# Kernel optimization log

Hardware: AMD Instinct MI355X
Metric: run time of the kernel (lower is better)

Reference implementation:

```python
import jax, jax.numpy as jnp
import numpy as np


def _safe_norm(x, eps=1e-8):
    return jnp.sqrt(jnp.clip(jnp.sum(x * x, axis=-1, keepdims=True), eps))


def _normalize(x, eps=1e-8):
    return x / _safe_norm(x, eps)


def _safe_direction(primary, fallback, eps=1e-6):
    bad = _safe_norm(primary, eps) < eps  # [N,1] bool
    out = jnp.where(bad, fallback, primary)
    return _normalize(out, eps)


def _build_frames(x):
    # x: [N,3] (N >= 2). Returns per-node rotation frames [N,3,3] (columns = axes).
    d = x[1:] - x[:-1]
    prev = jnp.concatenate([d[:1], d], axis=0)
    nxt = jnp.concatenate([d, d[-1:]], axis=0)
    tangent = _safe_direction(prev + nxt, nxt)
    curvature = _safe_direction(nxt - prev, prev)
    ay_raw = curvature - tangent * jnp.sum(curvature * tangent, axis=-1, keepdims=True)
    ay = _safe_direction(ay_raw, jnp.cross(tangent, prev))
    az = _safe_direction(jnp.cross(tangent, ay), jnp.cross(tangent, curvature))
    ay = _safe_direction(jnp.cross(az, tangent), ay)
    return jnp.stack([tangent, ay, az], axis=-1)


def setup_inputs() -> dict:
    key = jax.random.key(0)
    N, H, EH = 1024, 256, 128  # EH = max(16, H//2)
    ks = jax.random.split(key, 16)

    def lin(k, fi, fo):
        k1, k2 = jax.random.split(k)
        lim = 1.0 / np.sqrt(fi)
        W = jax.random.uniform(k1, (fi, fo), minval=-lim, maxval=lim, dtype=jnp.float32)
        b = jax.random.uniform(k2, (fo,), minval=-lim, maxval=lim, dtype=jnp.float32)
        return W, b

    h = jax.random.normal(ks[0], (N, H), dtype=jnp.float32)
    x_cond = jnp.cumsum(jax.random.normal(ks[1], (N, 3), dtype=jnp.float32) * 1.5, axis=0)
    x_t = x_cond + 0.05 * jax.random.normal(ks[2], (N, 3), dtype=jnp.float32)
    tau = jax.random.uniform(ks[3], (1,), dtype=jnp.float32)
    W_np1, b_np1 = lin(ks[4], H + 6, H)
    W_np2, b_np2 = lin(ks[5], H, H)
    w_src, b_src = lin(ks[6], H, 1)
    w_dst, b_dst = lin(ks[7], H, 1)
    w_ns, b_ns = lin(ks[8], H, 1)
    W_eg1, b_eg1 = lin(ks[9], 4, EH)
    w_eg2, b_eg2 = lin(ks[10], EH, 1)
    W_out1, b_out1 = lin(ks[11], H + 6, H)
    W_out2, b_out2 = lin(ks[12], H, 3)
    return dict(h=h, x_t=x_t, x_cond=x_cond, tau=tau,
                W_np1=W_np1, b_np1=b_np1, W_np2=W_np2, b_np2=b_np2,
                w_src=w_src, b_src=b_src, w_dst=w_dst, b_dst=b_dst,
                w_ns=w_ns, b_ns=b_ns, W_eg1=W_eg1, b_eg1=b_eg1,
                w_eg2=w_eg2, b_eg2=b_eg2, W_out1=W_out1, b_out1=b_out1,
                W_out2=W_out2, b_out2=b_out2)


def reference(h, x_t, x_cond, tau,
              W_np1, b_np1, W_np2, b_np2,
              w_src, b_src, w_dst, b_dst,
              w_ns, b_ns, W_eg1, b_eg1, w_eg2, b_eg2,
              W_out1, b_out1, W_out2, b_out2):
    silu = jax.nn.silu
    n = x_t.shape[0]
    frames = _build_frames(x_cond)                       # [N,3,3]
    delta = x_t - x_cond
    delta_local = jnp.einsum('nji,nj->ni', frames, delta)  # frames^T @ delta
    t = tau.reshape(())
    t_emb = jnp.broadcast_to(jnp.stack([t, jnp.sin(t), jnp.cos(t)]), (n, 3))
    node_feat = jnp.concatenate([h, delta_local, t_emb], axis=-1)
    nh = silu(node_feat @ W_np1 + b_np1)
    nh = silu(nh @ W_np2 + b_np2)                        # [N,H]
    # pairwise local geometry: rel[n,m] = x[m] - x[n], rotated into node n's frame
    rel = x_t[None, :, :] - x_t[:, None, :]              # [N,N,3]
    rel_local = jnp.einsum('nji,nmj->nmi', frames, rel)  # [N,N,3]
    dist = jnp.linalg.norm(rel_local, axis=-1, keepdims=True)
    edge_feat = jnp.concatenate([rel_local, dist], axis=-1)  # [N,N,4]
    eh = silu(edge_feat @ W_eg1 + b_eg1)                 # [N,N,EH]
    edge_logit = (eh @ w_eg2 + b_eg2)[..., 0]            # [N,N]
    src = nh @ w_src + b_src                             # [N,1] -> broadcast over m
    dst = (nh @ w_dst + b_dst)[:, 0]                     # [N]
    logits = src + dst[None, :] + edge_logit             # [N,N]
    diag = jnp.eye(n, dtype=bool)
    logits = jnp.where(diag, -10000.0, logits)
    attn = jax.nn.softmax(logits, axis=1)
    attn = jnp.where(diag, 0.0, attn)
    attn = attn / jnp.clip(jnp.sum(attn, axis=1, keepdims=True), 1e-6)
    ns = jax.nn.sigmoid(nh @ w_ns + b_ns)[:, 0]          # [N]
    msgs = jnp.einsum('nm,m,nmi->ni', attn, ns, rel_local)  # [N,3]
    uf = jnp.concatenate([nh, delta_local, msgs], axis=-1)
    local_update = silu(uf @ W_out1 + b_out1) @ W_out2 + b_out2
    vel_local = local_update + 0.25 * msgs
    return jnp.einsum('nij,nj->ni', frames, vel_local)
```

## Files before the change

kernel.cpp:

```cpp
#include <hip/hip_runtime.h>
#include <math.h>

#define DEV __device__ __forceinline__

typedef float v2f __attribute__((ext_vector_type(2)));
DEV v2f splat2(float s){ return (v2f){s, s}; }
DEV v2f pkfma(v2f a, v2f b, v2f c){ return __builtin_elementwise_fma(a, b, c); }

struct F3 { float x, y, z; };

DEV F3 mkf3(float x, float y, float z){ F3 r; r.x=x; r.y=y; r.z=z; return r; }
DEV F3 f3add(F3 a, F3 b){ return mkf3(a.x+b.x, a.y+b.y, a.z+b.z); }
DEV F3 f3sub(F3 a, F3 b){ return mkf3(a.x-b.x, a.y-b.y, a.z-b.z); }
DEV F3 f3scale(F3 a, float s){ return mkf3(a.x*s, a.y*s, a.z*s); }
DEV float f3dot(F3 a, F3 b){ return a.x*b.x + a.y*b.y + a.z*b.z; }
DEV F3 f3cross(F3 a, F3 b){
  return mkf3(a.y*b.z - a.z*b.y, a.z*b.x - a.x*b.z, a.x*b.y - a.y*b.x);
}
DEV F3 f3dir(F3 v){
  float ss = f3dot(v, v);
  float inv = 1.0f / sqrtf(fmaxf(ss, 1e-6f));
  return f3scale(v, inv);
}
DEV float fast_silu(float x){
  return x * __builtin_amdgcn_rcpf(1.0f + __expf(-x));
}
DEV float fast_sigmoid(float x){
  return __builtin_amdgcn_rcpf(1.0f + __expf(-x));
}

__global__ __launch_bounds__(256) void node_mlp(
    const float* __restrict__ h, const float* __restrict__ xc,
    const float* __restrict__ xt, const float* __restrict__ tau,
    const float* __restrict__ W1, const float* __restrict__ b1,
    const float* __restrict__ W2, const float* __restrict__ b2,
    const float* __restrict__ w_src, const float* __restrict__ b_src,
    const float* __restrict__ w_dst, const float* __restrict__ b_dst,
    const float* __restrict__ w_ns, const float* __restrict__ b_ns,
    const float* __restrict__ W_eg1, const float* __restrict__ b_eg1,
    const float* __restrict__ w_eg2,
    float* __restrict__ frames, float* __restrict__ dl,
    float* __restrict__ wpk,
    float* __restrict__ nh, float* __restrict__ srcv,
    float* __restrict__ dstv, float* __restrict__ nsv, int N)
{
  const int n0 = blockIdx.x * 4, tid = threadIdx.x;
  __shared__ float4 fA[262];
  __shared__ float4 fB[256];
  __shared__ float red[4][4][3];
  __shared__ float sdl[4][3];

  if (blockIdx.x == 0 && tid >= 128) {
    int j = tid - 128;
    const float nl2e = -1.44269504088896340736f;
    const float nln2 = -0.69314718055994530942f;
    wpk[j*8+0] = nl2e * W_eg1[j];
    wpk[j*8+1] = nl2e * W_eg1[128 + j];
    wpk[j*8+2] = nl2e * W_eg1[256 + j];
    wpk[j*8+3] = nl2e * W_eg1[384 + j];
    wpk[j*8+4] = nl2e * b_eg1[j];
    wpk[j*8+5] = nln2 * w_eg2[j];
    wpk[j*8+6] = 0.f; wpk[j*8+7] = 0.f;
    if (j < 16) wpk[1024 + j] = 0.f;
  }

  if (tid < 4) {
    int n = n0 + tid;
    int pn = (n > 0) ? n - 1 : 0;
    int qn = (n < N - 1) ? n : N - 2;
    F3 prev = mkf3(xc[(pn+1)*3+0]-xc[pn*3+0], xc[(pn+1)*3+1]-xc[pn*3+1], xc[(pn+1)*3+2]-xc[pn*3+2]);
    F3 nxt  = mkf3(xc[(qn+1)*3+0]-xc[qn*3+0], xc[(qn+1)*3+1]-xc[qn*3+1], xc[(qn+1)*3+2]-xc[qn*3+2]);

    F3 tangent = f3dir(f3add(prev, nxt));
    F3 curv    = f3dir(f3sub(nxt, prev));
    float ct   = f3dot(curv, tangent);
    F3 ay      = f3dir(f3sub(curv, f3scale(tangent, ct)));
    F3 az      = f3dir(f3cross(tangent, ay));
    ay         = f3dir(f3cross(az, tangent));

    float* fr = frames + n * 9;
    fr[0] = tangent.x; fr[1] = ay.x; fr[2] = az.x;
    fr[3] = tangent.y; fr[4] = ay.y; fr[5] = az.y;
    fr[6] = tangent.z; fr[7] = ay.z; fr[8] = az.z;

    F3 delta = mkf3(xt[n*3+0]-xc[n*3+0], xt[n*3+1]-xc[n*3+1], xt[n*3+2]-xc[n*3+2]);
    float d0 = f3dot(tangent, delta), d1 = f3dot(ay, delta), d2 = f3dot(az, delta);
    dl[n*3+0] = d0; dl[n*3+1] = d1; dl[n*3+2] = d2;
    sdl[tid][0] = d0; sdl[tid][1] = d1; sdl[tid][2] = d2;
  }
  __syncthreads();

  {
    const float* hp = h + n0 * 256 + tid;
    fA[tid] = make_float4(hp[0], hp[256], hp[512], hp[768]);
  }
  if (tid < 6) {
    int k = 256 + tid;
    float4 v;
    if (tid < 3) {
      v = make_float4(sdl[0][tid], sdl[1][tid], sdl[2][tid], sdl[3][tid]);
    } else {
      float t = tau[0];
      float s = (tid == 3) ? t : ((tid == 4) ? sinf(t) : cosf(t));
      v = make_float4(s, s, s, s);
    }
    fA[k] = v;
  }
  __syncthreads();

  {
    float bb = b1[tid];
    float a0 = bb, a1 = bb, a2 = bb, a3 = bb;
    const float* Wp = W1 + tid;
    for (int kb = 0; kb < 256; kb += 64) {
      float w[64];
      #pragma unroll
      for (int u = 0; u < 64; ++u) w[u] = Wp[(kb + u) * 256];
      #pragma unroll
      for (int u = 0; u < 64; ++u) {
        float4 f = fA[kb + u];
        a0 = fmaf(f.x, w[u], a0); a1 = fmaf(f.y, w[u], a1);
        a2 = fmaf(f.z, w[u], a2); a3 = fmaf(f.w, w[u], a3);
      }
    }
    #pragma unroll
    for (int k = 256; k < 262; ++k) {
      float w = Wp[k * 256];
      float4 f = fA[k];
      a0 = fmaf(f.x, w, a0); a1 = fmaf(f.y, w, a1);
      a2 = fmaf(f.z, w, a2); a3 = fmaf(f.w, w, a3);
    }
    fB[tid] = make_float4(fast_silu(a0), fast_silu(a1), fast_silu(a2), fast_silu(a3));
  }
  __syncthreads();

  float bb = b2[tid];
  float a0 = bb, a1 = bb, a2 = bb, a3 = bb;
  const float* Wp = W2 + tid;
  for (int kb = 0; kb < 256; kb += 64) {
    float w[64];
    #pragma unroll
    for (int u = 0; u < 64; ++u) w[u] = Wp[(kb + u) * 256];
    #pragma unroll
    for (int u = 0; u < 64; ++u) {
      float4 f = fB[kb + u];
      a0 = fmaf(f.x, w[u], a0); a1 = fmaf(f.y, w[u], a1);
      a2 = fmaf(f.z, w[u], a2); a3 = fmaf(f.w, w[u], a3);
    }
  }

  const float wsv = w_src[tid], wdv = w_dst[tid], wnv = w_ns[tid];
  const int wave = tid >> 6, lane = tid & 63;
  float va[4] = {fast_silu(a0), fast_silu(a1), fast_silu(a2), fast_silu(a3)};
  #pragma unroll
  for (int r = 0; r < 4; ++r) {
    nh[(n0 + r) * 256 + tid] = va[r];
    float ps = va[r] * wsv, pd = va[r] * wdv, pn = va[r] * wnv;
    for (int off = 32; off; off >>= 1) {
      ps += __shfl_down(ps, off);
      pd += __shfl_down(pd, off);
      pn += __shfl_down(pn, off);
    }
    if (lane == 0) { red[wave][r][0] = ps; red[wave][r][1] = pd; red[wave][r][2] = pn; }
  }
  __syncthreads();
  if (tid < 4) {
    int r = tid;
    float s0 = 0.f, s1 = 0.f, s2 = 0.f;
    #pragma unroll
    for (int w = 0; w < 4; ++w) { s0 += red[w][r][0]; s1 += red[w][r][1]; s2 += red[w][r][2]; }
    srcv[n0 + r] = s0 + b_src[0];
    dstv[n0 + r] = s1 + b_dst[0];
    nsv[n0 + r]  = fast_sigmoid(s2 + b_ns[0]);
  }
}

__global__ __launch_bounds__(256) void edge_softmax(
    const float* __restrict__ x_t, const float* __restrict__ frames,
    const float* __restrict__ srcv, const float* __restrict__ dstv,
    const float* __restrict__ nsv,
    const float* __restrict__ wpk, const float* __restrict__ b_eg2,
    float* __restrict__ msgs, int N)
{
  const int n = blockIdx.x, tid = threadIdx.x;
  __shared__ float redmax[4];
  __shared__ float red[4][4];

  const float f0 = frames[n*9+0], f1 = frames[n*9+1], f2 = frames[n*9+2],
              f3_ = frames[n*9+3], f4 = frames[n*9+4], f5 = frames[n*9+5],
              f6 = frames[n*9+6], f7 = frames[n*9+7], f8 = frames[n*9+8];
  const float x0 = x_t[n*3+0], x1 = x_t[n*3+1], x2 = x_t[n*3+2];
  const float sn = srcv[n];
  const float b2v = b_eg2[0];

  float r0s[4], r1s[4], r2s[4], dds[4], dst_r[4], ns_r[4];
  #pragma unroll
  for (int e = 0; e < 4; ++e) {
    const int m = e * 256 + tid;
    dst_r[e] = dstv[m];
    ns_r[e]  = nsv[m];
    float rx = x_t[m * 3 + 0] - x0;
    float ry = x_t[m * 3 + 1] - x1;
    float rz = x_t[m * 3 + 2] - x2;
    r0s[e] = f0 * rx + f3_ * ry + f6 * rz;
    r1s[e] = f1 * rx + f4 * ry + f7 * rz;
    r2s[e] = f2 * rx + f5 * ry + f8 * rz;
    dds[e] = sqrtf(r0s[e]*r0s[e] + r1s[e]*r1s[e] + r2s[e]*r2s[e]);
  }
  const v2f r0A = {r0s[0], r0s[1]}, r0B = {r0s[2], r0s[3]};
  const v2f r1A = {r1s[0], r1s[1]}, r1B = {r1s[2], r1s[3]};
  const v2f r2A = {r2s[0], r2s[1]}, r2B = {r2s[2], r2s[3]};
  const v2f ddA = {dds[0], dds[1]}, ddB = {dds[2], dds[3]};

  v2f accA = {0.f, 0.f}, accB = {0.f, 0.f};

  const float4* __restrict__ wp4 = (const float4*)wpk;

#define J_STEP(WA, WB)                                                        \
  {                                                                           \
    v2f wxx = splat2(WA.x), wyy = splat2(WA.y);                               \
    v2f wzz = splat2(WA.z), wdd = splat2(WA.w);                               \
    v2f wbb = splat2(WB.x), w22 = splat2(WB.y);                               \
    v2f tpA = pkfma(wdd, ddA, wbb);                                           \
    tpA = pkfma(wzz, r2A, tpA);                                               \
    tpA = pkfma(wyy, r1A, tpA);                                               \
    tpA = pkfma(wxx, r0A, tpA);                                               \
    v2f tpB = pkfma(wdd, ddB, wbb);                                           \
    tpB = pkfma(wzz, r2B, tpB);                                               \
    tpB = pkfma(wyy, r1B, tpB);                                               \
    tpB = pkfma(wxx, r0B, tpB);                                               \
    v2f eA, eB;                                                               \
    eA.x = __builtin_amdgcn_exp2f(tpA.x); eA.y = __builtin_amdgcn_exp2f(tpA.y); \
    eB.x = __builtin_amdgcn_exp2f(tpB.x); eB.y = __builtin_amdgcn_exp2f(tpB.y); \
    v2f opA = eA + splat2(1.0f);                                              \
    v2f opB = eB + splat2(1.0f);                                              \
    v2f sgA, sgB;                                                             \
    sgA.x = __builtin_amdgcn_rcpf(opA.x); sgA.y = __builtin_amdgcn_rcpf(opA.y); \
    sgB.x = __builtin_amdgcn_rcpf(opB.x); sgB.y = __builtin_amdgcn_rcpf(opB.y); \
    accA = pkfma(w22 * tpA, sgA, accA);                                       \
    accB = pkfma(w22 * tpB, sgB, accB);                                       \
  }

  float4 ca0 = wp4[0], cb0 = wp4[1], ca1 = wp4[2], cb1 = wp4[3];
  for (int c = 0; c < 64; ++c) {
    float4 na0 = wp4[(c + 1) * 4 + 0];
    float4 nb0 = wp4[(c + 1) * 4 + 1];
    float4 na1 = wp4[(c + 1) * 4 + 2];
    float4 nb1 = wp4[(c + 1) * 4 + 3];
    J_STEP(ca0, cb0)
    J_STEP(ca1, cb1)
    ca0 = na0; cb0 = nb0; ca1 = na1; cb1 = nb1;
  }
#undef J_STEP

  float l[4];
  float lmax = -3.4e38f;
  float accs[4] = {accA.x, accA.y, accB.x, accB.y};
  #pragma unroll
  for (int e = 0; e < 4; ++e) {
    const int m = e * 256 + tid;
    float lg = sn + dst_r[e] + b2v + accs[e];
    if (m == n) lg = -10000.0f;
    l[e] = lg;
    lmax = fmaxf(lmax, lg);
  }

  for (int off = 32; off; off >>= 1) lmax = fmaxf(lmax, __shfl_down(lmax, off));
  const int wave = tid >> 6, lane = tid & 63;
  if (lane == 0) redmax[wave] = lmax;
  __syncthreads();
  const float mx = fmaxf(fmaxf(redmax[0], redmax[1]), fmaxf(redmax[2], redmax[3]));

  float r0all[4] = {r0A.x, r0A.y, r0B.x, r0B.y};
  float r1all[4] = {r1A.x, r1A.y, r1B.x, r1B.y};
  float r2all[4] = {r2A.x, r2A.y, r2B.x, r2B.y};
  float sum = 0.f, a0 = 0.f, a1 = 0.f, a2 = 0.f;
  #pragma unroll
  for (int e = 0; e < 4; ++e) {
    float ee = __expf(l[e] - mx);
    sum += ee;
    float w = ee * ns_r[e];
    a0 = fmaf(w, r0all[e], a0);
    a1 = fmaf(w, r1all[e], a1);
    a2 = fmaf(w, r2all[e], a2);
  }
  for (int off = 32; off; off >>= 1) {
    sum += __shfl_down(sum, off);
    a0 += __shfl_down(a0, off);
    a1 += __shfl_down(a1, off);
    a2 += __shfl_down(a2, off);
  }
  if (lane == 0) { red[wave][0] = sum; red[wave][1] = a0; red[wave][2] = a1; red[wave][3] = a2; }
  __syncthreads();
  if (tid == 0) {
    float Z  = red[0][0] + red[1][0] + red[2][0] + red[3][0];
    float m0 = red[0][1] + red[1][1] + red[2][1] + red[3][1];
    float m1 = red[0][2] + red[1][2] + red[2][2] + red[3][2];
    float m2 = red[0][3] + red[1][3] + red[2][3] + red[3][3];
    float invZ = 1.0f / Z;
    msgs[n * 3 + 0] = m0 * invZ;
    msgs[n * 3 + 1] = m1 * invZ;
    msgs[n * 3 + 2] = m2 * invZ;
  }
}

__global__ __launch_bounds__(256) void out_mlp(
    const float* __restrict__ nh, const float* __restrict__ dl,
    const float* __restrict__ msgs, const float* __restrict__ frames,
    const float* __restrict__ W1, const float* __restrict__ b1,
    const float* __restrict__ W2, const float* __restrict__ b2,
    float* __restrict__ out, int N)
{
  const int n0 = blockIdx.x * 4, tid = threadIdx.x;
  __shared__ float4 feat4[262];
  __shared__ float red[4][4][3];
  {
    const float* hp = nh + n0 * 256 + tid;
    feat4[tid] = make_float4(hp[0], hp[256], hp[512], hp[768]);
  }
  if (tid < 6) {
    int k = 256 + tid;
    float4 v;
    if (tid < 3) {
      v = make_float4(dl[(n0+0)*3+tid], dl[(n0+1)*3+tid],
                      dl[(n0+2)*3+tid], dl[(n0+3)*3+tid]);
    } else {
      int c = tid - 3;
      v = make_float4(msgs[(n0+0)*3+c], msgs[(n0+1)*3+c],
                      msgs[(n0+2)*3+c], msgs[(n0+3)*3+c]);
    }
    feat4[k] = v;
  }
  __syncthreads();

  float bb = b1[tid];
  float a0 = bb, a1 = bb, a2 = bb, a3 = bb;
  const float* Wp = W1 + tid;
  for (int kb = 0; kb < 256; kb += 64) {
    float w[64];
    #pragma unroll
    for (int u = 0; u < 64; ++u) w[u] = Wp[(kb + u) * 256];
    #pragma unroll
    for (int u = 0; u < 64; ++u) {
      float4 f = feat4[kb + u];
      a0 = fmaf(f.x, w[u], a0); a1 = fmaf(f.y, w[u], a1);
      a2 = fmaf(f.z, w[u], a2); a3 = fmaf(f.w, w[u], a3);
    }
  }
  #pragma unroll
  for (int k = 256; k < 262; ++k) {
    float w = Wp[k * 256];
    float4 f = feat4[k];
    a0 = fmaf(f.x, w, a0); a1 = fmaf(f.y, w, a1);
    a2 = fmaf(f.z, w, a2); a3 = fmaf(f.w, w, a3);
  }

  const float w0 = W2[tid * 3 + 0], w1 = W2[tid * 3 + 1], w2 = W2[tid * 3 + 2];
  const int wave = tid >> 6, lane = tid & 63;
  float va[4] = {fast_silu(a0), fast_silu(a1), fast_silu(a2), fast_silu(a3)};
  #pragma unroll
  for (int r = 0; r < 4; ++r) {
    float p0 = va[r] * w0, p1 = va[r] * w1, p2 = va[r] * w2;
    for (int off = 32; off; off >>= 1) {
      p0 += __shfl_down(p0, off);
      p1 += __shfl_down(p1, off);
      p2 += __shfl_down(p2, off);
    }
    if (lane == 0) { red[wave][r][0] = p0; red[wave][r][1] = p1; red[wave][r][2] = p2; }
  }
  __syncthreads();
  if (tid < 4) {
    int r = tid, n = n0 + r;
    float s0 = 0.f, s1 = 0.f, s2 = 0.f;
    #pragma unroll
    for (int w = 0; w < 4; ++w) { s0 += red[w][r][0]; s1 += red[w][r][1]; s2 += red[w][r][2]; }
    float m0 = msgs[n * 3 + 0], m1 = msgs[n * 3 + 1], m2 = msgs[n * 3 + 2];
    float v0 = s0 + b2[0] + 0.25f * m0;
    float v1 = s1 + b2[1] + 0.25f * m1;
    float v2 = s2 + b2[2] + 0.25f * m2;
    const float* fr = frames + n * 9;
    out[n * 3 + 0] = fr[0] * v0 + fr[1] * v1 + fr[2] * v2;
    out[n * 3 + 1] = fr[3] * v0 + fr[4] * v1 + fr[5] * v2;
    out[n * 3 + 2] = fr[6] * v0 + fr[7] * v1 + fr[8] * v2;
  }
}

extern "C" void kernel_launch(void* const* d_in, const int* in_sizes, int n_in,
                              void* d_out, int out_size, void* d_ws, size_t ws_size,
                              hipStream_t stream) {
  const float* h      = (const float*)d_in[0];
  const float* x_t    = (const float*)d_in[1];
  const float* x_cond = (const float*)d_in[2];
  const float* tau    = (const float*)d_in[3];
  const float* W_np1  = (const float*)d_in[4];
  const float* b_np1  = (const float*)d_in[5];
  const float* W_np2  = (const float*)d_in[6];
  const float* b_np2  = (const float*)d_in[7];
  const float* w_src  = (const float*)d_in[8];
  const float* b_src  = (const float*)d_in[9];
  const float* w_dst  = (const float*)d_in[10];
  const float* b_dst  = (const float*)d_in[11];
  const float* w_ns   = (const float*)d_in[12];
  const float* b_ns   = (const float*)d_in[13];
  const float* W_eg1  = (const float*)d_in[14];
  const float* b_eg1  = (const float*)d_in[15];
  const float* w_eg2  = (const float*)d_in[16];
  const float* b_eg2  = (const float*)d_in[17];
  const float* W_out1 = (const float*)d_in[18];
  const float* b_out1 = (const float*)d_in[19];
  const float* W_out2 = (const float*)d_in[20];
  const float* b_out2 = (const float*)d_in[21];
  float* out = (float*)d_out;

  const int N = in_sizes[1] / 3;

  float* ws     = (float*)d_ws;
  float* frames = ws;
  float* dl     = frames + N * 9;
  float* nh     = dl + N * 3;
  float* srcv   = nh + N * 256;
  float* dstv   = srcv + N;
  float* nsv    = dstv + N;
  float* msgs   = nsv + N;
  float* wpk    = msgs + N * 3;

  node_mlp<<<N / 4, 256, 0, stream>>>(h, x_cond, x_t, tau,
                                      W_np1, b_np1, W_np2, b_np2,
                                      w_src, b_src, w_dst, b_dst, w_ns, b_ns,
                                      W_eg1, b_eg1, w_eg2,
                                      frames, dl, wpk,
                                      nh, srcv, dstv, nsv, N);
  edge_softmax<<<N, 256, 0, stream>>>(x_t, frames, srcv, dstv, nsv,
                                      wpk, b_eg2, msgs, N);
  out_mlp<<<N / 4, 256, 0, stream>>>(nh, dl, msgs, frames,
                                     W_out1, b_out1, W_out2, b_out2, out, N);
}
```

Before: 61.93 us.

## Fuse output MLP into edge softmax kernel and approximate SiLU with polynomial

```diff
diff --git a/kernel.cpp b/kernel.cpp
--- a/kernel.cpp
+++ b/kernel.cpp
@@ -2,10 +2,6 @@
 #include <math.h>
 
 #define DEV __device__ __forceinline__
-
-typedef float v2f __attribute__((ext_vector_type(2)));
-DEV v2f splat2(float s){ return (v2f){s, s}; }
-DEV v2f pkfma(v2f a, v2f b, v2f c){ return __builtin_elementwise_fma(a, b, c); }
 
 struct F3 { float x, y, z; };
 
@@ -175,23 +171,30 @@
   }
 }
 
-__global__ __launch_bounds__(256) void edge_softmax(
+__global__ __launch_bounds__(256, 4) void edge_out(
     const float* __restrict__ x_t, const float* __restrict__ frames,
     const float* __restrict__ srcv, const float* __restrict__ dstv,
     const float* __restrict__ nsv,
     const float* __restrict__ wpk, const float* __restrict__ b_eg2,
-    float* __restrict__ msgs, int N)
+    const float* __restrict__ nh, const float* __restrict__ dl,
+    const float* __restrict__ W_o1, const float* __restrict__ b_o1,
+    const float* __restrict__ W_o2, const float* __restrict__ b_o2,
+    float* __restrict__ out, int N)
 {
   const int n = blockIdx.x, tid = threadIdx.x;
   __shared__ float redmax[4];
   __shared__ float red[4][4];
+  __shared__ float redo[4][3];
+  __shared__ __align__(16) float uf[264];
 
   const float f0 = frames[n*9+0], f1 = frames[n*9+1], f2 = frames[n*9+2],
               f3_ = frames[n*9+3], f4 = frames[n*9+4], f5 = frames[n*9+5],
               f6 = frames[n*9+6], f7 = frames[n*9+7], f8 = frames[n*9+8];
   const float x0 = x_t[n*3+0], x1 = x_t[n*3+1], x2 = x_t[n*3+2];
-  const float sn = srcv[n];
-  const float b2v = b_eg2[0];
+  const float sn2 = srcv[n] + b_eg2[0];
+
+  const float fl_nh = nh[n * 256 + tid];
+  const float fl_dl = (tid < 3) ? dl[n * 3 + tid] : 0.f;
 
   float r0s[4], r1s[4], r2s[4], dds[4], dst_r[4], ns_r[4];
   #pragma unroll
@@ -207,38 +210,26 @@
     r2s[e] = f2 * rx + f5 * ry + f8 * rz;
     dds[e] = sqrtf(r0s[e]*r0s[e] + r1s[e]*r1s[e] + r2s[e]*r2s[e]);
   }
-  const v2f r0A = {r0s[0], r0s[1]}, r0B = {r0s[2], r0s[3]};
-  const v2f r1A = {r1s[0], r1s[1]}, r1B = {r1s[2], r1s[3]};
-  const v2f r2A = {r2s[0], r2s[1]}, r2B = {r2s[2], r2s[3]};
-  const v2f ddA = {dds[0], dds[1]}, ddB = {dds[2], dds[3]};
-
-  v2f accA = {0.f, 0.f}, accB = {0.f, 0.f};
 
   const float4* __restrict__ wp4 = (const float4*)wpk;
-
-#define J_STEP(WA, WB)                                                        \
-  {                                                                           \
-    v2f wxx = splat2(WA.x), wyy = splat2(WA.y);                               \
-    v2f wzz = splat2(WA.z), wdd = splat2(WA.w);                               \
-    v2f wbb = splat2(WB.x), w22 = splat2(WB.y);                               \
-    v2f tpA = pkfma(wdd, ddA, wbb);                                           \
-    tpA = pkfma(wzz, r2A, tpA);                                               \
-    tpA = pkfma(wyy, r1A, tpA);                                               \
-    tpA = pkfma(wxx, r0A, tpA);                                               \
-    v2f tpB = pkfma(wdd, ddB, wbb);                                           \
-    tpB = pkfma(wzz, r2B, tpB);                                               \
-    tpB = pkfma(wyy, r1B, tpB);                                               \
-    tpB = pkfma(wxx, r0B, tpB);                                               \
-    v2f eA, eB;                                                               \
-    eA.x = __builtin_amdgcn_exp2f(tpA.x); eA.y = __builtin_amdgcn_exp2f(tpA.y); \
-    eB.x = __builtin_amdgcn_exp2f(tpB.x); eB.y = __builtin_amdgcn_exp2f(tpB.y); \
-    v2f opA = eA + splat2(1.0f);                                              \
-    v2f opB = eB + splat2(1.0f);                                              \
-    v2f sgA, sgB;                                                             \
-    sgA.x = __builtin_amdgcn_rcpf(opA.x); sgA.y = __builtin_amdgcn_rcpf(opA.y); \
-    sgB.x = __builtin_amdgcn_rcpf(opB.x); sgB.y = __builtin_amdgcn_rcpf(opB.y); \
-    accA = pkfma(w22 * tpA, sgA, accA);                                       \
-    accB = pkfma(w22 * tpB, sgB, accB);                                       \
+  const float P0 = 0.991384f, P1 = -0.818352f, P2c = 0.333072f;
+  float acc[4] = {0.f, 0.f, 0.f, 0.f};
+
+#define J_STEP(WA, WB)                                                  \
+  {                                                                     \
+    _Pragma("unroll")                                                   \
+    for (int e = 0; e < 4; ++e) {                                       \
+      float tp = fmaf(WA.w, dds[e], WB.x);                              \
+      tp = fmaf(WA.z, r2s[e], tp);                                      \
+      tp = fmaf(WA.y, r1s[e], tp);                                      \
+      tp = fmaf(WA.x, r0s[e], tp);                                      \
+      float xe = __builtin_amdgcn_exp2f(-fabsf(tp));      \
+      float p2 = fmaf(fmaf(P2c, xe, P1), xe, P0);                       \
+      float v  = (xe * tp) * p2;                          \
+      float u  = tp - v;                                 \
+      float mn = fminf(u, v);                                           \
+      acc[e] = fmaf(WB.y, mn, acc[e]);         \
+    }                                                                   \
   }
 
   float4 ca0 = wp4[0], cb0 = wp4[1], ca1 = wp4[2], cb1 = wp4[3];
@@ -255,11 +246,10 @@
 
   float l[4];
   float lmax = -3.4e38f;
-  float accs[4] = {accA.x, accA.y, accB.x, accB.y};
   #pragma unroll
   for (int e = 0; e < 4; ++e) {
     const int m = e * 256 + tid;
-    float lg = sn + dst_r[e] + b2v + accs[e];
+    float lg = sn2 + dst_r[e] + acc[e];
     if (m == n) lg = -10000.0f;
     l[e] = lg;
     lmax = fmaxf(lmax, lg);
@@ -271,18 +261,15 @@
   __syncthreads();
   const float mx = fmaxf(fmaxf(redmax[0], redmax[1]), fmaxf(redmax[2], redmax[3]));
 
-  float r0all[4] = {r0A.x, r0A.y, r0B.x, r0B.y};
-  float r1all[4] = {r1A.x, r1A.y, r1B.x, r1B.y};
-  float r2all[4] = {r2A.x, r2A.y, r2B.x, r2B.y};
   float sum = 0.f, a0 = 0.f, a1 = 0.f, a2 = 0.f;
   #pragma unroll
   for (int e = 0; e < 4; ++e) {
     float ee = __expf(l[e] - mx);
     sum += ee;
     float w = ee * ns_r[e];
-    a0 = fmaf(w, r0all[e], a0);
-    a1 = fmaf(w, r1all[e], a1);
-    a2 = fmaf(w, r2all[e], a2);
+    a0 = fmaf(w, r0s[e], a0);
+    a1 = fmaf(w, r1s[e], a1);
+    a2 = fmaf(w, r2s[e], a2);
   }
   for (int off = 32; off; off >>= 1) {
     sum += __shfl_down(sum, off);
@@ -291,6 +278,9 @@
     a2 += __shfl_down(a2, off);
   }
   if (lane == 0) { red[wave][0] = sum; red[wave][1] = a0; red[wave][2] = a1; red[wave][3] = a2; }
+
+  uf[tid] = fl_nh;
+  if (tid < 3) uf[256 + tid] = fl_dl;
   __syncthreads();
   if (tid == 0) {
     float Z  = red[0][0] + red[1][0] + red[2][0] + red[3][0];
@@ -298,90 +288,50 @@
     float m1 = red[0][2] + red[1][2] + red[2][2] + red[3][2];
     float m2 = red[0][3] + red[1][3] + red[2][3] + red[3][3];
     float invZ = 1.0f / Z;
-    msgs[n * 3 + 0] = m0 * invZ;
-    msgs[n * 3 + 1] = m1 * invZ;
-    msgs[n * 3 + 2] = m2 * invZ;
-  }
-}
-
-__global__ __launch_bounds__(256) void out_mlp(
-    const float* __restrict__ nh, const float* __restrict__ dl,
-    const float* __restrict__ msgs, const float* __restrict__ frames,
-    const float* __restrict__ W1, const float* __restrict__ b1,
-    const float* __restrict__ W2, const float* __restrict__ b2,
-    float* __restrict__ out, int N)
-{
-  const int n0 = blockIdx.x * 4, tid = threadIdx.x;
-  __shared__ float4 feat4[262];
-  __shared__ float red[4][4][3];
-  {
-    const float* hp = nh + n0 * 256 + tid;
-    feat4[tid] = make_float4(hp[0], hp[256], hp[512], hp[768]);
-  }
-  if (tid < 6) {
-    int k = 256 + tid;
-    float4 v;
-    if (tid < 3) {
-      v = make_float4(dl[(n0+0)*3+tid], dl[(n0+1)*3+tid],
-                      dl[(n0+2)*3+tid], dl[(n0+3)*3+tid]);
-    } else {
-      int c = tid - 3;
-      v = make_float4(msgs[(n0+0)*3+c], msgs[(n0+1)*3+c],
-                      msgs[(n0+2)*3+c], msgs[(n0+3)*3+c]);
-    }
-    feat4[k] = v;
-  }
-  __syncthreads();
-
-  float bb = b1[tid];
-  float a0 = bb, a1 = bb, a2 = bb, a3 = bb;
-  const float* Wp = W1 + tid;
-  for (int kb = 0; kb < 256; kb += 64) {
-    float w[64];
-    #pragma unroll
-    for (int u = 0; u < 64; ++u) w[u] = Wp[(kb + u) * 256];
-    #pragma unroll
-    for (int u = 0; u < 64; ++u) {
-      float4 f = feat4[kb + u];
-      a0 = fmaf(f.x, w[u], a0); a1 = fmaf(f.y, w[u], a1);
-      a2 = fmaf(f.z, w[u], a2); a3 = fmaf(f.w, w[u], a3);
-    }
-  }
-  #pragma unroll
-  for (int k = 256; k < 262; ++k) {
-    float w = Wp[k * 256];
-    float4 f = feat4[k];
-    a0 = fmaf(f.x, w, a0); a1 = fmaf(f.y, w, a1);
-    a2 = fmaf(f.z, w, a2); a3 = fmaf(f.w, w, a3);
-  }
-
-  const float w0 = W2[tid * 3 + 0], w1 = W2[tid * 3 + 1], w2 = W2[tid * 3 + 2];
-  const int wave = tid >> 6, lane = tid & 63;
-  float va[4] = {fast_silu(a0), fast_silu(a1), fast_silu(a2), fast_silu(a3)};
-  #pragma unroll
-  for (int r = 0; r < 4; ++r) {
-    float p0 = va[r] * w0, p1 = va[r] * w1, p2 = va[r] * w2;
-    for (int off = 32; off; off >>= 1) {
-      p0 += __shfl_down(p0, off);
-      p1 += __shfl_down(p1, off);
-      p2 += __shfl_down(p2, off);
-    }
-    if (lane == 0) { red[wave][r][0] = p0; red[wave][r][1] = p1; red[wave][r][2] = p2; }
-  }
-  __syncthreads();
-  if (tid < 4) {
-    int r = tid, n = n0 + r;
-    float s0 = 0.f, s1 = 0.f, s2 = 0.f;
-    #pragma unroll
-    for (int w = 0; w < 4; ++w) { s0 += red[w][r][0]; s1 += red[w][r][1]; s2 += red[w][r][2]; }
-    float m0 = msgs[n * 3 + 0], m1 = msgs[n * 3 + 1], m2 = msgs[n * 3 + 2];
-    float v0 = s0 + b2[0] + 0.25f * m0;
-    float v1 = s1 + b2[1] + 0.25f * m1;
-    float v2 = s2 + b2[2] + 0.25f * m2;
-    const float* fr = frames + n * 9;
-    out[n * 3 + 0] = fr[0] * v0 + fr[1] * v1 + fr[2] * v2;
-    out[n * 3 + 1] = fr[3] * v0 + fr[4] * v1 + fr[5] * v2;
-    out[n * 3 + 2] = fr[6] * v0 + fr[7] * v1 + fr[8] * v2;
+    uf[259] = m0 * invZ; uf[260] = m1 * invZ; uf[261] = m2 * invZ;
+    uf[262] = 0.f; uf[263] = 0.f;
+  }
+  __syncthreads();
+
+  const float4* uf4 = (const float4*)uf;
+  float acc_o = b_o1[tid];
+  const float* Wp = W_o1 + tid;
+  for (int kb = 0; kb < 256; kb += 32) {
+    float w[32];
+    #pragma unroll
+    for (int u = 0; u < 32; ++u) w[u] = Wp[(kb + u) * 256];
+    #pragma unroll
+    for (int u = 0; u < 32; u += 4) {
+      float4 f = uf4[(kb + u) >> 2];
+      acc_o = fmaf(f.x, w[u+0], acc_o);
+      acc_o = fmaf(f.y, w[u+1], acc_o);
+      acc_o = fmaf(f.z, w[u+2], acc_o);
+      acc_o = fmaf(f.w, w[u+3], acc_o);
+    }
+  }
+  #pragma unroll
+  for (int k = 256; k < 262; ++k) acc_o = fmaf(uf[k], Wp[k * 256], acc_o);
+
+  float hid = fast_silu(acc_o);
+  const float w0 = W_o2[tid * 3 + 0], w1 = W_o2[tid * 3 + 1], w2 = W_o2[tid * 3 + 2];
+  float p0 = hid * w0, p1 = hid * w1, p2 = hid * w2;
+  for (int off = 32; off; off >>= 1) {
+    p0 += __shfl_down(p0, off);
+    p1 += __shfl_down(p1, off);
+    p2 += __shfl_down(p2, off);
+  }
+  if (lane == 0) { redo[wave][0] = p0; redo[wave][1] = p1; redo[wave][2] = p2; }
+  __syncthreads();
+  if (tid == 0) {
+    float s0 = redo[0][0] + redo[1][0] + redo[2][0] + redo[3][0];
+    float s1 = redo[0][1] + redo[1][1] + redo[2][1] + redo[3][1];
+    float s2 = redo[0][2] + redo[1][2] + redo[2][2] + redo[3][2];
+    float v0 = s0 + b_o2[0] + 0.25f * uf[259];
+    float v1 = s1 + b_o2[1] + 0.25f * uf[260];
+    float v2 = s2 + b_o2[2] + 0.25f * uf[261];
+    out[n * 3 + 0] = f0 * v0 + f1 * v1 + f2 * v2;
+    out[n * 3 + 1] = f3_ * v0 + f4 * v1 + f5 * v2;
+    out[n * 3 + 2] = f6 * v0 + f7 * v1 + f8 * v2;
   }
 }
 
@@ -421,8 +371,7 @@
   float* srcv   = nh + N * 256;
   float* dstv   = srcv + N;
   float* nsv    = dstv + N;
-  float* msgs   = nsv + N;
-  float* wpk    = msgs + N * 3;
+  float* wpk    = nsv + N;
 
   node_mlp<<<N / 4, 256, 0, stream>>>(h, x_cond, x_t, tau,
                                       W_np1, b_np1, W_np2, b_np2,
@@ -430,8 +379,7 @@
                                       W_eg1, b_eg1, w_eg2,
                                       frames, dl, wpk,
                                       nh, srcv, dstv, nsv, N);
-  edge_softmax<<<N, 256, 0, stream>>>(x_t, frames, srcv, dstv, nsv,
-                                      wpk, b_eg2, msgs, N);
-  out_mlp<<<N / 4, 256, 0, stream>>>(nh, dl, msgs, frames,
-                                     W_out1, b_out1, W_out2, b_out2, out, N);
-}
+  edge_out<<<N, 256, 0, stream>>>(x_t, frames, srcv, dstv, nsv,
+                                  wpk, b_eg2, nh, dl,
+                                  W_out1, b_out1, W_out2, b_out2, out, N);
+}
```

New measurement: 67.13 us. 8.4% more time.

## Remap node and output MLPs to one row per wave with float4 weight loads

Applied to the files above, without the earlier changes.

```diff
diff --git a/kernel.cpp b/kernel.cpp
--- a/kernel.cpp
+++ b/kernel.cpp
@@ -29,7 +29,7 @@
   return __builtin_amdgcn_rcpf(1.0f + __expf(-x));
 }
 
-__global__ __launch_bounds__(256) void node_mlp(
+__global__ __launch_bounds__(256, 1) void node_mlp(
     const float* __restrict__ h, const float* __restrict__ xc,
     const float* __restrict__ xt, const float* __restrict__ tau,
     const float* __restrict__ W1, const float* __restrict__ b1,
@@ -45,9 +45,12 @@
     float* __restrict__ dstv, float* __restrict__ nsv, int N)
 {
   const int n0 = blockIdx.x * 4, tid = threadIdx.x;
-  __shared__ float4 fA[262];
-  __shared__ float4 fB[256];
-  __shared__ float red[4][4][3];
+  const int row = tid >> 6, lane = tid & 63;
+  const int c4 = lane << 2;
+  const int n = n0 + row;
+
+  __shared__ __align__(16) float feat[4][264];
+  __shared__ __align__(16) float fB[4][264];
   __shared__ float sdl[4][3];
 
   if (blockIdx.x == 0 && tid >= 128) {
@@ -65,9 +68,9 @@
   }
 
   if (tid < 4) {
-    int n = n0 + tid;
-    int pn = (n > 0) ? n - 1 : 0;
-    int qn = (n < N - 1) ? n : N - 2;
+    int nn = n0 + tid;
+    int pn = (nn > 0) ? nn - 1 : 0;
+    int qn = (nn < N - 1) ? nn : N - 2;
     F3 prev = mkf3(xc[(pn+1)*3+0]-xc[pn*3+0], xc[(pn+1)*3+1]-xc[pn*3+1], xc[(pn+1)*3+2]-xc[pn*3+2]);
     F3 nxt  = mkf3(xc[(qn+1)*3+0]-xc[qn*3+0], xc[(qn+1)*3+1]-xc[qn*3+1], xc[(qn+1)*3+2]-xc[qn*3+2]);
 
@@ -78,100 +81,96 @@
     F3 az      = f3dir(f3cross(tangent, ay));
     ay         = f3dir(f3cross(az, tangent));
 
-    float* fr = frames + n * 9;
+    float* fr = frames + nn * 9;
     fr[0] = tangent.x; fr[1] = ay.x; fr[2] = az.x;
     fr[3] = tangent.y; fr[4] = ay.y; fr[5] = az.y;
     fr[6] = tangent.z; fr[7] = ay.z; fr[8] = az.z;
 
-    F3 delta = mkf3(xt[n*3+0]-xc[n*3+0], xt[n*3+1]-xc[n*3+1], xt[n*3+2]-xc[n*3+2]);
+    F3 delta = mkf3(xt[nn*3+0]-xc[nn*3+0], xt[nn*3+1]-xc[nn*3+1], xt[nn*3+2]-xc[nn*3+2]);
     float d0 = f3dot(tangent, delta), d1 = f3dot(ay, delta), d2 = f3dot(az, delta);
-    dl[n*3+0] = d0; dl[n*3+1] = d1; dl[n*3+2] = d2;
+    dl[nn*3+0] = d0; dl[nn*3+1] = d1; dl[nn*3+2] = d2;
     sdl[tid][0] = d0; sdl[tid][1] = d1; sdl[tid][2] = d2;
   }
   __syncthreads();
 
+  *(float4*)(&feat[row][c4]) = *(const float4*)(h + n * 256 + c4);
+  if (lane == 0) {
+    float t = tau[0];
+    feat[row][256] = sdl[row][0];
+    feat[row][257] = sdl[row][1];
+    feat[row][258] = sdl[row][2];
+    feat[row][259] = t;
+    feat[row][260] = sinf(t);
+    feat[row][261] = cosf(t);
+    feat[row][262] = 0.f; feat[row][263] = 0.f;
+  }
+  __syncthreads();
+
+  const float4* __restrict__ W1v = (const float4*)W1;
+  float4 acc = *(const float4*)(b1 + c4);
+  for (int kb = 0; kb < 256; kb += 32) {
+    float4 w[32];
+    #pragma unroll
+    for (int u = 0; u < 32; ++u) w[u] = W1v[(kb + u) * 64 + lane];
+    #pragma unroll
+    for (int u = 0; u < 32; ++u) {
+      float f = feat[row][kb + u];
+      acc.x = fmaf(f, w[u].x, acc.x);
+      acc.y = fmaf(f, w[u].y, acc.y);
+      acc.z = fmaf(f, w[u].z, acc.z);
+      acc.w = fmaf(f, w[u].w, acc.w);
+    }
+  }
+  #pragma unroll
+  for (int k = 256; k < 262; ++k) {
+    float4 w = W1v[k * 64 + lane];
+    float f = feat[row][k];
+    acc.x = fmaf(f, w.x, acc.x);
+    acc.y = fmaf(f, w.y, acc.y);
+    acc.z = fmaf(f, w.z, acc.z);
+    acc.w = fmaf(f, w.w, acc.w);
+  }
   {
-    const float* hp = h + n0 * 256 + tid;
-    fA[tid] = make_float4(hp[0], hp[256], hp[512], hp[768]);
-  }
-  if (tid < 6) {
-    int k = 256 + tid;
-    float4 v;
-    if (tid < 3) {
-      v = make_float4(sdl[0][tid], sdl[1][tid], sdl[2][tid], sdl[3][tid]);
-    } else {
-      float t = tau[0];
-      float s = (tid == 3) ? t : ((tid == 4) ? sinf(t) : cosf(t));
-      v = make_float4(s, s, s, s);
+    float4 v1 = make_float4(fast_silu(acc.x), fast_silu(acc.y),
+                            fast_silu(acc.z), fast_silu(acc.w));
+    *(float4*)(&fB[row][c4]) = v1;
+  }
+  __syncthreads();
+
+  const float4* __restrict__ W2v = (const float4*)W2;
+  float4 a2 = *(const float4*)(b2 + c4);
+  for (int kb = 0; kb < 256; kb += 32) {
+    float4 w[32];
+    #pragma unroll
+    for (int u = 0; u < 32; ++u) w[u] = W2v[(kb + u) * 64 + lane];
+    #pragma unroll
+    for (int u = 0; u < 32; ++u) {
+      float f = fB[row][kb + u];
+      a2.x = fmaf(f, w[u].x, a2.x);
+      a2.y = fmaf(f, w[u].y, a2.y);
+      a2.z = fmaf(f, w[u].z, a2.z);
+      a2.w = fmaf(f, w[u].w, a2.w);
     }
-    fA[k] = v;
-  }
-  __syncthreads();
-
-  {
-    float bb = b1[tid];
-    float a0 = bb, a1 = bb, a2 = bb, a3 = bb;
-    const float* Wp = W1 + tid;
-    for (int kb = 0; kb < 256; kb += 64) {
-      float w[64];
-      #pragma unroll
-      for (int u = 0; u < 64; ++u) w[u] = Wp[(kb + u) * 256];
-      #pragma unroll
-      for (int u = 0; u < 64; ++u) {
-        float4 f = fA[kb + u];
-        a0 = fmaf(f.x, w[u], a0); a1 = fmaf(f.y, w[u], a1);
-        a2 = fmaf(f.z, w[u], a2); a3 = fmaf(f.w, w[u], a3);
-      }
-    }
-    #pragma unroll
-    for (int k = 256; k < 262; ++k) {
-      float w = Wp[k * 256];
-      float4 f = fA[k];
-      a0 = fmaf(f.x, w, a0); a1 = fmaf(f.y, w, a1);
-      a2 = fmaf(f.z, w, a2); a3 = fmaf(f.w, w, a3);
-    }
-    fB[tid] = make_float4(fast_silu(a0), fast_silu(a1), fast_silu(a2), fast_silu(a3));
-  }
-  __syncthreads();
-
-  float bb = b2[tid];
-  float a0 = bb, a1 = bb, a2 = bb, a3 = bb;
-  const float* Wp = W2 + tid;
-  for (int kb = 0; kb < 256; kb += 64) {
-    float w[64];
-    #pragma unroll
-    for (int u = 0; u < 64; ++u) w[u] = Wp[(kb + u) * 256];
-    #pragma unroll
-    for (int u = 0; u < 64; ++u) {
-      float4 f = fB[kb + u];
-      a0 = fmaf(f.x, w[u], a0); a1 = fmaf(f.y, w[u], a1);
-      a2 = fmaf(f.z, w[u], a2); a3 = fmaf(f.w, w[u], a3);
-    }
-  }
-
-  const float wsv = w_src[tid], wdv = w_dst[tid], wnv = w_ns[tid];
-  const int wave = tid >> 6, lane = tid & 63;
-  float va[4] = {fast_silu(a0), fast_silu(a1), fast_silu(a2), fast_silu(a3)};
-  #pragma unroll
-  for (int r = 0; r < 4; ++r) {
-    nh[(n0 + r) * 256 + tid] = va[r];
-    float ps = va[r] * wsv, pd = va[r] * wdv, pn = va[r] * wnv;
-    for (int off = 32; off; off >>= 1) {
-      ps += __shfl_down(ps, off);
-      pd += __shfl_down(pd, off);
-      pn += __shfl_down(pn, off);
-    }
-    if (lane == 0) { red[wave][r][0] = ps; red[wave][r][1] = pd; red[wave][r][2] = pn; }
-  }
-  __syncthreads();
-  if (tid < 4) {
-    int r = tid;
-    float s0 = 0.f, s1 = 0.f, s2 = 0.f;
-    #pragma unroll
-    for (int w = 0; w < 4; ++w) { s0 += red[w][r][0]; s1 += red[w][r][1]; s2 += red[w][r][2]; }
-    srcv[n0 + r] = s0 + b_src[0];
-    dstv[n0 + r] = s1 + b_dst[0];
-    nsv[n0 + r]  = fast_sigmoid(s2 + b_ns[0]);
+  }
+  float4 va = make_float4(fast_silu(a2.x), fast_silu(a2.y),
+                          fast_silu(a2.z), fast_silu(a2.w));
+  *(float4*)(&nh[n * 256 + c4]) = va;
+
+  float4 ws4 = *(const float4*)(w_src + c4);
+  float4 wd4 = *(const float4*)(w_dst + c4);
+  float4 wn4 = *(const float4*)(w_ns + c4);
+  float ps = va.x*ws4.x + va.y*ws4.y + va.z*ws4.z + va.w*ws4.w;
+  float pd = va.x*wd4.x + va.y*wd4.y + va.z*wd4.z + va.w*wd4.w;
+  float pn = va.x*wn4.x + va.y*wn4.y + va.z*wn4.z + va.w*wn4.w;
+  for (int off = 32; off; off >>= 1) {
+    ps += __shfl_down(ps, off);
+    pd += __shfl_down(pd, off);
+    pn += __shfl_down(pn, off);
+  }
+  if (lane == 0) {
+    srcv[n] = ps + b_src[0];
+    dstv[n] = pd + b_dst[0];
+    nsv[n]  = fast_sigmoid(pn + b_ns[0]);
   }
 }
 
@@ -304,7 +303,7 @@
   }
 }
 
-__global__ __launch_bounds__(256) void out_mlp(
+__global__ __launch_bounds__(256, 1) void out_mlp(
     const float* __restrict__ nh, const float* __restrict__ dl,
     const float* __restrict__ msgs, const float* __restrict__ frames,
     const float* __restrict__ W1, const float* __restrict__ b1,
@@ -312,72 +311,67 @@
     float* __restrict__ out, int N)
 {
   const int n0 = blockIdx.x * 4, tid = threadIdx.x;
-  __shared__ float4 feat4[262];
-  __shared__ float red[4][4][3];
-  {
-    const float* hp = nh + n0 * 256 + tid;
-    feat4[tid] = make_float4(hp[0], hp[256], hp[512], hp[768]);
-  }
-  if (tid < 6) {
-    int k = 256 + tid;
-    float4 v;
-    if (tid < 3) {
-      v = make_float4(dl[(n0+0)*3+tid], dl[(n0+1)*3+tid],
-                      dl[(n0+2)*3+tid], dl[(n0+3)*3+tid]);
-    } else {
-      int c = tid - 3;
-      v = make_float4(msgs[(n0+0)*3+c], msgs[(n0+1)*3+c],
-                      msgs[(n0+2)*3+c], msgs[(n0+3)*3+c]);
-    }
-    feat4[k] = v;
-  }
-  __syncthreads();
-
-  float bb = b1[tid];
-  float a0 = bb, a1 = bb, a2 = bb, a3 = bb;
-  const float* Wp = W1 + tid;
-  for (int kb = 0; kb < 256; kb += 64) {
-    float w[64];
-    #pragma unroll
-    for (int u = 0; u < 64; ++u) w[u] = Wp[(kb + u) * 256];
-    #pragma unroll
-    for (int u = 0; u < 64; ++u) {
-      float4 f = feat4[kb + u];
-      a0 = fmaf(f.x, w[u], a0); a1 = fmaf(f.y, w[u], a1);
-      a2 = fmaf(f.z, w[u], a2); a3 = fmaf(f.w, w[u], a3);
+  const int row = tid >> 6, lane = tid & 63;
+  const int c4 = lane << 2;
+  const int n = n0 + row;
+
+  __shared__ __align__(16) float feat[4][264];
+
+  *(float4*)(&feat[row][c4]) = *(const float4*)(nh + n * 256 + c4);
+  if (lane == 0) {
+    feat[row][256] = dl[n*3+0];
+    feat[row][257] = dl[n*3+1];
+    feat[row][258] = dl[n*3+2];
+    feat[row][259] = msgs[n*3+0];
+    feat[row][260] = msgs[n*3+1];
+    feat[row][261] = msgs[n*3+2];
+    feat[row][262] = 0.f; feat[row][263] = 0.f;
+  }
+  __syncthreads();
+
+  const float4* __restrict__ W1v = (const float4*)W1;
+  float4 acc = *(const float4*)(b1 + c4);
+  for (int kb = 0; kb < 256; kb += 32) {
+    float4 w[32];
+    #pragma unroll
+    for (int u = 0; u < 32; ++u) w[u] = W1v[(kb + u) * 64 + lane];
+    #pragma unroll
+    for (int u = 0; u < 32; ++u) {
+      float f = feat[row][kb + u];
+      acc.x = fmaf(f, w[u].x, acc.x);
+      acc.y = fmaf(f, w[u].y, acc.y);
+      acc.z = fmaf(f, w[u].z, acc.z);
+      acc.w = fmaf(f, w[u].w, acc.w);
     }
   }
   #pragma unroll
   for (int k = 256; k < 262; ++k) {
-    float w = Wp[k * 256];
-    float4 f = feat4[k];
-    a0 = fmaf(f.x, w, a0); a1 = fmaf(f.y, w, a1);
-    a2 = fmaf(f.z, w, a2); a3 = fmaf(f.w, w, a3);
-  }
-
-  const float w0 = W2[tid * 3 + 0], w1 = W2[tid * 3 + 1], w2 = W2[tid * 3 + 2];
-  const int wave = tid >> 6, lane = tid & 63;
-  float va[4] = {fast_silu(a0), fast_silu(a1), fast_silu(a2), fast_silu(a3)};
-  #pragma unroll
-  for (int r = 0; r < 4; ++r) {
-    float p0 = va[r] * w0, p1 = va[r] * w1, p2 = va[r] * w2;
-    for (int off = 32; off; off >>= 1) {
-      p0 += __shfl_down(p0, off);
-      p1 += __shfl_down(p1, off);
-      p2 += __shfl_down(p2, off);
-    }
-    if (lane == 0) { red[wave][r][0] = p0; red[wave][r][1] = p1; red[wave][r][2] = p2; }
-  }
-  __syncthreads();
-  if (tid < 4) {
-    int r = tid, n = n0 + r;
-    float s0 = 0.f, s1 = 0.f, s2 = 0.f;
-    #pragma unroll
-    for (int w = 0; w < 4; ++w) { s0 += red[w][r][0]; s1 += red[w][r][1]; s2 += red[w][r][2]; }
-    float m0 = msgs[n * 3 + 0], m1 = msgs[n * 3 + 1], m2 = msgs[n * 3 + 2];
-    float v0 = s0 + b2[0] + 0.25f * m0;
-    float v1 = s1 + b2[1] + 0.25f * m1;
-    float v2 = s2 + b2[2] + 0.25f * m2;
+    float4 w = W1v[k * 64 + lane];
+    float f = feat[row][k];
+    acc.x = fmaf(f, w.x, acc.x);
+    acc.y = fmaf(f, w.y, acc.y);
+    acc.z = fmaf(f, w.z, acc.z);
+    acc.w = fmaf(f, w.w, acc.w);
+  }
+  float4 hid = make_float4(fast_silu(acc.x), fast_silu(acc.y),
+                           fast_silu(acc.z), fast_silu(acc.w));
+
+  const float4* __restrict__ W2v = (const float4*)W2;
+  float4 q0 = W2v[lane * 3 + 0];
+  float4 q1 = W2v[lane * 3 + 1];
+  float4 q2 = W2v[lane * 3 + 2];
+  float p0 = hid.x*q0.x + hid.y*q0.w + hid.z*q1.z + hid.w*q2.y;
+  float p1 = hid.x*q0.y + hid.y*q1.x + hid.z*q1.w + hid.w*q2.z;
+  float p2 = hid.x*q0.z + hid.y*q1.y + hid.z*q2.x + hid.w*q2.w;
+  for (int off = 32; off; off >>= 1) {
+    p0 += __shfl_down(p0, off);
+    p1 += __shfl_down(p1, off);
+    p2 += __shfl_down(p2, off);
+  }
+  if (lane == 0) {
+    float v0 = p0 + b2[0] + 0.25f * feat[row][259];
+    float v1 = p1 + b2[1] + 0.25f * feat[row][260];
+    float v2 = p2 + b2[2] + 0.25f * feat[row][261];
     const float* fr = frames + n * 9;
     out[n * 3 + 0] = fr[0] * v0 + fr[1] * v1 + fr[2] * v2;
     out[n * 3 + 1] = fr[3] * v0 + fr[4] * v1 + fr[5] * v2;
```

Result: slower. 69.74 us (+12.6%).
